# Performance work log

Hardware: AMD Instinct MI355X
Metric: run time of the kernel (lower is better)

## Reference

```python
import jax, jax.numpy as jnp
import numpy as np

N_NODES = 50000
N_EDGES = 800000
IN_DIM = 64
EDGE_DIM = 32
OUT_DIM = 64


def setup_inputs() -> dict:
    key = jax.random.key(0)
    ks = jax.random.split(key, 7)
    x = jax.random.normal(ks[0], (N_NODES, IN_DIM), dtype=jnp.float32)
    edge_index = jax.random.randint(ks[1], (2, N_EDGES), 0, N_NODES, dtype=jnp.int64)
    edge_attr = jax.random.normal(ks[2], (N_EDGES, EDGE_DIM), dtype=jnp.float32)
    scale_msg = 1.0 / np.sqrt(IN_DIM + EDGE_DIM)
    scale_self = 1.0 / np.sqrt(IN_DIM)
    msg_w = jax.random.normal(ks[3], (IN_DIM + EDGE_DIM, OUT_DIM), dtype=jnp.float32) * scale_msg
    msg_b = jax.random.normal(ks[4], (OUT_DIM,), dtype=jnp.float32) * scale_msg
    self_w = jax.random.normal(ks[5], (IN_DIM, OUT_DIM), dtype=jnp.float32) * scale_self
    self_b = jax.random.normal(ks[6], (OUT_DIM,), dtype=jnp.float32) * scale_self
    return {"x": x, "edge_index": edge_index, "edge_attr": edge_attr,
            "msg_w": msg_w, "msg_b": msg_b, "self_w": self_w, "self_b": self_b}


def reference(x, edge_index, edge_attr, msg_w, msg_b, self_w, self_b):
    src = edge_index[0]
    dst = edge_index[1]
    n = x.shape[0]
    # gather source features, concat edge attrs, message linear: [E, out]
    msg_in = jnp.concatenate([x[src], edge_attr], axis=1)
    messages = msg_in @ msg_w + msg_b
    # scatter-mean over destination nodes
    agg = jax.ops.segment_sum(messages, dst, num_segments=n)
    deg = jax.ops.segment_sum(jnp.ones((dst.shape[0],), dtype=x.dtype), dst, num_segments=n)
    deg = jnp.maximum(deg, 1.0)[:, None]
    agg = agg / deg
    return x @ self_w + self_b + agg
```

## Files before the change

### kernel.cpp

```cpp
#include <hip/hip_runtime.h>


constexpr int N_NODES  = 50000;
constexpr int N_EDGES  = 800000;
constexpr int IN_DIM   = 64;
constexpr int EDGE_DIM = 32;
constexpr int OUT_DIM  = 64;
constexpr int CAP      = 48;
constexpr int OVF_CAP  = 65536;

__device__ __forceinline__ void place_one(int dst, int e, int src,
                                          int* cnt, int2* buckets,
                                          int4* ovf, int* ovf_cur) {
    const int pos = atomicAdd(&cnt[dst], 1);
    if (pos < CAP) {
        buckets[(size_t)dst * CAP + pos] = make_int2(e, src);
    } else {
        const int o = atomicAdd(ovf_cur, 1);
        if (o < OVF_CAP) ovf[o] = make_int4(dst, e, src, 0);
    }
}

__global__ __launch_bounds__(256) void place_bucket_k(
    const int* __restrict__ ei, int* cnt, int2* __restrict__ buckets,
    int4* __restrict__ ovf, int* ovf_cur)
{
    const int t = blockIdx.x * 256 + threadIdx.x;
    if (t * 4 + 3 < N_EDGES) {
        const int4 d4 = ((const int4*)(ei + N_EDGES))[t];
        const int4 s4 = ((const int4*)ei)[t];
        place_one(d4.x, 4 * t + 0, s4.x, cnt, buckets, ovf, ovf_cur);
        place_one(d4.y, 4 * t + 1, s4.y, cnt, buckets, ovf, ovf_cur);
        place_one(d4.z, 4 * t + 2, s4.z, cnt, buckets, ovf, ovf_cur);
        place_one(d4.w, 4 * t + 3, s4.w, cnt, buckets, ovf, ovf_cur);
    } else {
        for (int e = t * 4; e < min(t * 4 + 4, N_EDGES); ++e)
            place_one(ei[N_EDGES + e], e, ei[e], cnt, buckets, ovf, ovf_cur);
    }
}

__global__ __launch_bounds__(256) void aggregate_bucket_k(
    const float* __restrict__ x, const float* __restrict__ ea,
    const int2* __restrict__ buckets, const int* __restrict__ cnt,
    const int4* __restrict__ ovf, const int* __restrict__ ovf_cur,
    float* __restrict__ sum_x, float* __restrict__ sum_ea)
{
    const int lane   = threadIdx.x & 63;
    const int wave   = (blockIdx.x * blockDim.x + threadIdx.x) >> 6;
    const int nwaves = (gridDim.x * blockDim.x) >> 6;

    const int grpx = lane >> 4, colx = lane & 15;
    const int grpe = lane >> 3, cole = lane & 7;

    for (int n0 = wave * 2; n0 < N_NODES; n0 += nwaves * 2) {
        const int  nA   = __builtin_amdgcn_readfirstlane(n0);
        const bool hasB = (n0 + 1 < N_NODES);
        const int  nB   = nA + 1;

        const int cFA = __builtin_amdgcn_readfirstlane(cnt[nA]);
        const int cFB = hasB ? __builtin_amdgcn_readfirstlane(cnt[nB]) : 0;
        const int cA  = min(cFA, CAP);
        const int cB  = min(cFB, CAP);

        int eA = 0, srcA = 0, eB = 0, srcB = 0;
        if (lane < cA) { const int2 p = buckets[(size_t)nA * CAP + lane]; eA = p.x; srcA = p.y; }
        if (lane < cB) { const int2 p = buckets[(size_t)nB * CAP + lane]; eB = p.x; srcB = p.y; }

        float4 axA = {0,0,0,0}, aeA = {0,0,0,0};
        float4 axB = {0,0,0,0}, aeB = {0,0,0,0};

        const int mMax = max(cA, cB);
        for (int j = 0; j < mMax; j += 4) {
            const int jj  = j + grpx;
            const int sjA = __shfl(srcA, jj);
            const int sjB = __shfl(srcB, jj);
            if (jj < cA) {
                const float4 v = ((const float4*)(x + (size_t)sjA * IN_DIM))[colx];
                axA.x += v.x; axA.y += v.y; axA.z += v.z; axA.w += v.w;
            }
            if (jj < cB) {
                const float4 v = ((const float4*)(x + (size_t)sjB * IN_DIM))[colx];
                axB.x += v.x; axB.y += v.y; axB.z += v.z; axB.w += v.w;
            }
        }
        for (int j = 0; j < mMax; j += 8) {
            const int jj  = j + grpe;
            const int ejA = __shfl(eA, jj);
            const int ejB = __shfl(eB, jj);
            if (jj < cA) {
                const float4 v = ((const float4*)(ea + (size_t)ejA * EDGE_DIM))[cole];
                aeA.x += v.x; aeA.y += v.y; aeA.z += v.z; aeA.w += v.w;
            }
            if (jj < cB) {
                const float4 v = ((const float4*)(ea + (size_t)ejB * EDGE_DIM))[cole];
                aeB.x += v.x; aeB.y += v.y; aeB.z += v.z; aeB.w += v.w;
            }
        }

        if (cFA > CAP || cFB > CAP) {
            const int novf = min(__builtin_amdgcn_readfirstlane(*ovf_cur), OVF_CAP);
            for (int i = 0; i < novf; ++i) {
                const int4 v = ovf[i];
                const bool mA = (v.x == nA), mB = hasB && (v.x == nB);
                if (mA || mB) {
                    if (grpx == 0) {
                        const float4 t = ((const float4*)(x + (size_t)v.z * IN_DIM))[colx];
                        if (mA) { axA.x += t.x; axA.y += t.y; axA.z += t.z; axA.w += t.w; }
                        else    { axB.x += t.x; axB.y += t.y; axB.z += t.z; axB.w += t.w; }
                    }
                    if (grpe == 0) {
                        const float4 t = ((const float4*)(ea + (size_t)v.y * EDGE_DIM))[cole];
                        if (mA) { aeA.x += t.x; aeA.y += t.y; aeA.z += t.z; aeA.w += t.w; }
                        else    { aeB.x += t.x; aeB.y += t.y; aeB.z += t.z; aeB.w += t.w; }
                    }
                }
            }
        }

#pragma unroll
        for (int mask = 16; mask < 64; mask <<= 1) {
            axA.x += __shfl_xor(axA.x, mask); axA.y += __shfl_xor(axA.y, mask);
            axA.z += __shfl_xor(axA.z, mask); axA.w += __shfl_xor(axA.w, mask);
            axB.x += __shfl_xor(axB.x, mask); axB.y += __shfl_xor(axB.y, mask);
            axB.z += __shfl_xor(axB.z, mask); axB.w += __shfl_xor(axB.w, mask);
        }
#pragma unroll
        for (int mask = 8; mask < 64; mask <<= 1) {
            aeA.x += __shfl_xor(aeA.x, mask); aeA.y += __shfl_xor(aeA.y, mask);
            aeA.z += __shfl_xor(aeA.z, mask); aeA.w += __shfl_xor(aeA.w, mask);
            aeB.x += __shfl_xor(aeB.x, mask); aeB.y += __shfl_xor(aeB.y, mask);
            aeB.z += __shfl_xor(aeB.z, mask); aeB.w += __shfl_xor(aeB.w, mask);
        }

        if (lane < 16) ((float4*)(sum_x + (size_t)nA * IN_DIM))[lane] = axA;
        if (lane < 8)  ((float4*)(sum_ea + (size_t)nA * EDGE_DIM))[lane] = aeA;
        if (hasB) {
            if (lane < 16) ((float4*)(sum_x + (size_t)nB * IN_DIM))[lane] = axB;
            if (lane < 8)  ((float4*)(sum_ea + (size_t)nB * EDGE_DIM))[lane] = aeB;
        }
    }
}

__global__ __launch_bounds__(64) void finalize64_k(
    const float* __restrict__ x, const float* sum_x_in,
    const float* __restrict__ sum_ea, const int* __restrict__ cnt,
    const float* __restrict__ msg_w, const float* __restrict__ msg_b,
    const float* __restrict__ self_w, const float* __restrict__ self_b,
    float* out)
{
    const int c = threadIdx.x;

    float wm[96];
    float wsf[64];
#pragma unroll
    for (int k = 0; k < 96; ++k) wm[k] = msg_w[k * OUT_DIM + c];
#pragma unroll
    for (int k = 0; k < 64; ++k) wsf[k] = self_w[k * OUT_DIM + c];
    const float mb = msg_b[c];
    const float sb = self_b[c];

    for (int n0 = blockIdx.x; n0 < N_NODES; n0 += gridDim.x) {
        const int n = __builtin_amdgcn_readfirstlane(n0);

        const float4* r1 = (const float4*)(sum_x_in + (size_t)n * IN_DIM);
        const float4* r2 = (const float4*)(sum_ea   + (size_t)n * EDGE_DIM);
        const float4* r3 = (const float4*)(x        + (size_t)n * IN_DIM);
        const int d = cnt[n];

        float am0 = 0.f, am1 = 0.f, am2 = 0.f, am3 = 0.f;
        float as0 = 0.f, as1 = 0.f, as2 = 0.f, as3 = 0.f;
#pragma unroll
        for (int q = 0; q < 16; ++q) {
            const float4 v = r1[q];
            am0 = fmaf(v.x, wm[4 * q + 0], am0);
            am1 = fmaf(v.y, wm[4 * q + 1], am1);
            am2 = fmaf(v.z, wm[4 * q + 2], am2);
            am3 = fmaf(v.w, wm[4 * q + 3], am3);
        }
#pragma unroll
        for (int q = 0; q < 8; ++q) {
            const float4 v = r2[q];
            am0 = fmaf(v.x, wm[64 + 4 * q + 0], am0);
            am1 = fmaf(v.y, wm[64 + 4 * q + 1], am1);
            am2 = fmaf(v.z, wm[64 + 4 * q + 2], am2);
            am3 = fmaf(v.w, wm[64 + 4 * q + 3], am3);
        }
#pragma unroll
        for (int q = 0; q < 16; ++q) {
            const float4 v = r3[q];
            as0 = fmaf(v.x, wsf[4 * q + 0], as0);
            as1 = fmaf(v.y, wsf[4 * q + 1], as1);
            as2 = fmaf(v.z, wsf[4 * q + 2], as2);
            as3 = fmaf(v.w, wsf[4 * q + 3], as3);
        }

        const float inv  = 1.0f / (float)max(d, 1);
        const float bsel = (d > 0) ? 1.0f : 0.0f;
        const float am   = (am0 + am1) + (am2 + am3);
        const float as   = (as0 + as1) + (as2 + as3);

        out[(size_t)n * OUT_DIM + c] = as + sb + am * inv + mb * bsel;
    }
}

__global__ __launch_bounds__(768) void scatter_fb_k(
    const float* __restrict__ x, const int* __restrict__ ei,
    const float* __restrict__ ea, float* sum_x, float* sum_ea, int* deg)
{
    const int t  = threadIdx.x;
    const int el = t / 96;
    const int k  = t - el * 96;
    const int e  = blockIdx.x * 8 + el;
    if (e >= N_EDGES) return;
    const int dst = ei[N_EDGES + e];
    if (k < IN_DIM) {
        const int src = ei[e];
        atomicAdd(&sum_x[dst * IN_DIM + k], x[src * IN_DIM + k]);
        if (k == 0) atomicAdd(&deg[dst], 1);
    } else {
        const int kk = k - IN_DIM;
        atomicAdd(&sum_ea[dst * EDGE_DIM + kk], ea[e * EDGE_DIM + kk]);
    }
}

extern "C" void kernel_launch(void* const* d_in, const int* in_sizes, int n_in,
                              void* d_out, int out_size, void* d_ws, size_t ws_size,
                              hipStream_t stream) {
    const float* x      = (const float*)d_in[0];
    const int*   ei     = (const int*)d_in[1];
    const float* ea     = (const float*)d_in[2];
    const float* msg_w  = (const float*)d_in[3];
    const float* msg_b  = (const float*)d_in[4];
    const float* self_w = (const float*)d_in[5];
    const float* self_b = (const float*)d_in[6];

    float* out = (float*)d_out;

    int*   cnt     = (int*)d_ws;
    int*   ovf_cur = cnt + N_NODES;
    int2*  buckets = (int2*)(cnt + N_NODES + 16);
    int4*  ovf     = (int4*)(buckets + (size_t)N_NODES * CAP);
    float* sum_ea  = (float*)(ovf + OVF_CAP);
    const size_t need_bucket =
        ((size_t)N_NODES + 16 + 2 * (size_t)N_NODES * CAP + 4 * (size_t)OVF_CAP +
         (size_t)N_NODES * EDGE_DIM) * sizeof(int);

    if (ws_size >= need_bucket) {
        hipMemsetAsync(cnt, 0, (N_NODES + 16) * sizeof(int), stream);
        place_bucket_k<<<(N_EDGES / 4 + 255) / 256, 256, 0, stream>>>(
            ei, cnt, buckets, ovf, ovf_cur);
        aggregate_bucket_k<<<(N_NODES / 2 + 3) / 4, 256, 0, stream>>>(
            x, ea, buckets, cnt, ovf, ovf_cur, out, sum_ea);
        finalize64_k<<<4096, 64, 0, stream>>>(
            x, out, sum_ea, cnt, msg_w, msg_b, self_w, self_b, out);
    } else {
        float* fb_sum_ea = (float*)d_ws;
        int*   deg       = (int*)(fb_sum_ea + (size_t)N_NODES * EDGE_DIM);
        hipMemsetAsync(d_out, 0, (size_t)N_NODES * OUT_DIM * sizeof(float), stream);
        hipMemsetAsync(d_ws, 0, (size_t)N_NODES * (EDGE_DIM + 1) * sizeof(float), stream);
        scatter_fb_k<<<(N_EDGES + 7) / 8, 768, 0, stream>>>(
            x, ei, ea, out, fb_sum_ea, deg);
        finalize64_k<<<4096, 64, 0, stream>>>(
            x, out, fb_sum_ea, deg, msg_w, msg_b, self_w, self_b, out);
    }
}
```

Before: 299.3 us.

## Restructure aggregation to one node per wave with batched gathers, prefetch in finalize

```diff
diff --git a/kernel.cpp b/kernel.cpp
--- a/kernel.cpp
+++ b/kernel.cpp
@@ -8,6 +8,13 @@
 constexpr int OUT_DIM  = 64;
 constexpr int CAP      = 48;
 constexpr int OVF_CAP  = 65536;
+
+using vf4 = __attribute__((ext_vector_type(4))) float;
+using vi2 = __attribute__((ext_vector_type(2))) int;
+
+__device__ __forceinline__ float rl(float v, int srclane) {
+    return __int_as_float(__builtin_amdgcn_readlane(__float_as_int(v), srclane));
+}
 
 __device__ __forceinline__ void place_one(int dst, int e, int src,
                                           int* cnt, int2* buckets,
@@ -39,167 +46,190 @@
     }
 }
 
-__global__ __launch_bounds__(256) void aggregate_bucket_k(
+__global__ __launch_bounds__(256) void aggregate1_k(
     const float* __restrict__ x, const float* __restrict__ ea,
     const int2* __restrict__ buckets, const int* __restrict__ cnt,
     const int4* __restrict__ ovf, const int* __restrict__ ovf_cur,
     float* __restrict__ sum_x, float* __restrict__ sum_ea)
 {
-    const int lane   = threadIdx.x & 63;
-    const int wave   = (blockIdx.x * blockDim.x + threadIdx.x) >> 6;
-    const int nwaves = (gridDim.x * blockDim.x) >> 6;
+    const int lane = threadIdx.x & 63;
+    const int wave = (blockIdx.x * blockDim.x + threadIdx.x) >> 6;
+    if (wave >= N_NODES) return;
+    const int n = __builtin_amdgcn_readfirstlane(wave);
+
+    const vi2 p = __builtin_nontemporal_load(
+        (const vi2*)buckets + (size_t)n * CAP + lane);
+    const int cF = __builtin_amdgcn_readfirstlane(cnt[n]);
+    const int c  = min(cF, CAP);
+    const int e0 = p.x, s0 = p.y;
 
     const int grpx = lane >> 4, colx = lane & 15;
     const int grpe = lane >> 3, cole = lane & 7;
 
-    for (int n0 = wave * 2; n0 < N_NODES; n0 += nwaves * 2) {
-        const int  nA   = __builtin_amdgcn_readfirstlane(n0);
-        const bool hasB = (n0 + 1 < N_NODES);
-        const int  nB   = nA + 1;
-
-        const int cFA = __builtin_amdgcn_readfirstlane(cnt[nA]);
-        const int cFB = hasB ? __builtin_amdgcn_readfirstlane(cnt[nB]) : 0;
-        const int cA  = min(cFA, CAP);
-        const int cB  = min(cFB, CAP);
-
-        int eA = 0, srcA = 0, eB = 0, srcB = 0;
-        if (lane < cA) { const int2 p = buckets[(size_t)nA * CAP + lane]; eA = p.x; srcA = p.y; }
-        if (lane < cB) { const int2 p = buckets[(size_t)nB * CAP + lane]; eB = p.x; srcB = p.y; }
-
-        float4 axA = {0,0,0,0}, aeA = {0,0,0,0};
-        float4 axB = {0,0,0,0}, aeB = {0,0,0,0};
-
-        const int mMax = max(cA, cB);
-        for (int j = 0; j < mMax; j += 4) {
-            const int jj  = j + grpx;
-            const int sjA = __shfl(srcA, jj);
-            const int sjB = __shfl(srcB, jj);
-            if (jj < cA) {
-                const float4 v = ((const float4*)(x + (size_t)sjA * IN_DIM))[colx];
-                axA.x += v.x; axA.y += v.y; axA.z += v.z; axA.w += v.w;
+    vf4 xt[12], et[6];
+#pragma unroll
+    for (int i = 0; i < 12; ++i) xt[i] = (vf4){0, 0, 0, 0};
+#pragma unroll
+    for (int i = 0; i < 6; ++i) et[i] = (vf4){0, 0, 0, 0};
+
+#pragma unroll
+    for (int i = 0; i < 4; ++i) {
+        const int jj = 4 * i + grpx;
+        const int s  = __shfl(s0, jj);
+        if (jj < c) xt[i] = ((const vf4*)(x + (size_t)s * IN_DIM))[colx];
+    }
+#pragma unroll
+    for (int i = 0; i < 2; ++i) {
+        const int jj = 8 * i + grpe;
+        const int e  = __shfl(e0, jj);
+        if (jj < c) et[i] = __builtin_nontemporal_load(
+            (const vf4*)(ea + (size_t)e * EDGE_DIM) + cole);
+    }
+    if (c > 16) {
+#pragma unroll
+        for (int i = 4; i < 8; ++i) {
+            const int jj = 4 * i + grpx;
+            const int s  = __shfl(s0, jj);
+            if (jj < c) xt[i] = ((const vf4*)(x + (size_t)s * IN_DIM))[colx];
+        }
+#pragma unroll
+        for (int i = 2; i < 4; ++i) {
+            const int jj = 8 * i + grpe;
+            const int e  = __shfl(e0, jj);
+            if (jj < c) et[i] = __builtin_nontemporal_load(
+                (const vf4*)(ea + (size_t)e * EDGE_DIM) + cole);
+        }
+    }
+    if (c > 32) {
+#pragma unroll
+        for (int i = 8; i < 12; ++i) {
+            const int jj = 4 * i + grpx;
+            const int s  = __shfl(s0, jj);
+            if (jj < c) xt[i] = ((const vf4*)(x + (size_t)s * IN_DIM))[colx];
+        }
+#pragma unroll
+        for (int i = 4; i < 6; ++i) {
+            const int jj = 8 * i + grpe;
+            const int e  = __shfl(e0, jj);
+            if (jj < c) et[i] = __builtin_nontemporal_load(
+                (const vf4*)(ea + (size_t)e * EDGE_DIM) + cole);
+        }
+    }
+
+    vf4 ax = ((xt[0] + xt[1]) + (xt[2] + xt[3])) +
+             ((xt[4] + xt[5]) + (xt[6] + xt[7])) +
+             ((xt[8] + xt[9]) + (xt[10] + xt[11]));
+    vf4 ae = ((et[0] + et[1]) + (et[2] + et[3])) + (et[4] + et[5]);
+
+    if (cF > CAP) {
+        const int novf = min(__builtin_amdgcn_readfirstlane(*ovf_cur), OVF_CAP);
+        for (int i = 0; i < novf; ++i) {
+            const int4 v = ovf[i];
+            if (v.x == n) {
+                if (grpx == 0)
+                    ax += ((const vf4*)(x + (size_t)v.z * IN_DIM))[colx];
+                if (grpe == 0)
+                    ae += ((const vf4*)(ea + (size_t)v.y * EDGE_DIM))[cole];
             }
-            if (jj < cB) {
-                const float4 v = ((const float4*)(x + (size_t)sjB * IN_DIM))[colx];
-                axB.x += v.x; axB.y += v.y; axB.z += v.z; axB.w += v.w;
-            }
-        }
-        for (int j = 0; j < mMax; j += 8) {
-            const int jj  = j + grpe;
-            const int ejA = __shfl(eA, jj);
-            const int ejB = __shfl(eB, jj);
-            if (jj < cA) {
-                const float4 v = ((const float4*)(ea + (size_t)ejA * EDGE_DIM))[cole];
-                aeA.x += v.x; aeA.y += v.y; aeA.z += v.z; aeA.w += v.w;
-            }
-            if (jj < cB) {
-                const float4 v = ((const float4*)(ea + (size_t)ejB * EDGE_DIM))[cole];
-                aeB.x += v.x; aeB.y += v.y; aeB.z += v.z; aeB.w += v.w;
-            }
-        }
-
-        if (cFA > CAP || cFB > CAP) {
-            const int novf = min(__builtin_amdgcn_readfirstlane(*ovf_cur), OVF_CAP);
-            for (int i = 0; i < novf; ++i) {
-                const int4 v = ovf[i];
-                const bool mA = (v.x == nA), mB = hasB && (v.x == nB);
-                if (mA || mB) {
-                    if (grpx == 0) {
-                        const float4 t = ((const float4*)(x + (size_t)v.z * IN_DIM))[colx];
-                        if (mA) { axA.x += t.x; axA.y += t.y; axA.z += t.z; axA.w += t.w; }
-                        else    { axB.x += t.x; axB.y += t.y; axB.z += t.z; axB.w += t.w; }
-                    }
-                    if (grpe == 0) {
-                        const float4 t = ((const float4*)(ea + (size_t)v.y * EDGE_DIM))[cole];
-                        if (mA) { aeA.x += t.x; aeA.y += t.y; aeA.z += t.z; aeA.w += t.w; }
-                        else    { aeB.x += t.x; aeB.y += t.y; aeB.z += t.z; aeB.w += t.w; }
-                    }
-                }
-            }
-        }
-
-#pragma unroll
-        for (int mask = 16; mask < 64; mask <<= 1) {
-            axA.x += __shfl_xor(axA.x, mask); axA.y += __shfl_xor(axA.y, mask);
-            axA.z += __shfl_xor(axA.z, mask); axA.w += __shfl_xor(axA.w, mask);
-            axB.x += __shfl_xor(axB.x, mask); axB.y += __shfl_xor(axB.y, mask);
-            axB.z += __shfl_xor(axB.z, mask); axB.w += __shfl_xor(axB.w, mask);
-        }
-#pragma unroll
-        for (int mask = 8; mask < 64; mask <<= 1) {
-            aeA.x += __shfl_xor(aeA.x, mask); aeA.y += __shfl_xor(aeA.y, mask);
-            aeA.z += __shfl_xor(aeA.z, mask); aeA.w += __shfl_xor(aeA.w, mask);
-            aeB.x += __shfl_xor(aeB.x, mask); aeB.y += __shfl_xor(aeB.y, mask);
-            aeB.z += __shfl_xor(aeB.z, mask); aeB.w += __shfl_xor(aeB.w, mask);
-        }
-
-        if (lane < 16) ((float4*)(sum_x + (size_t)nA * IN_DIM))[lane] = axA;
-        if (lane < 8)  ((float4*)(sum_ea + (size_t)nA * EDGE_DIM))[lane] = aeA;
-        if (hasB) {
-            if (lane < 16) ((float4*)(sum_x + (size_t)nB * IN_DIM))[lane] = axB;
-            if (lane < 8)  ((float4*)(sum_ea + (size_t)nB * EDGE_DIM))[lane] = aeB;
-        }
-    }
-}
-
-__global__ __launch_bounds__(64) void finalize64_k(
+        }
+    }
+
+#pragma unroll
+    for (int mask = 16; mask < 64; mask <<= 1) {
+        ax.x += __shfl_xor(ax.x, mask); ax.y += __shfl_xor(ax.y, mask);
+        ax.z += __shfl_xor(ax.z, mask); ax.w += __shfl_xor(ax.w, mask);
+    }
+#pragma unroll
+    for (int mask = 8; mask < 64; mask <<= 1) {
+        ae.x += __shfl_xor(ae.x, mask); ae.y += __shfl_xor(ae.y, mask);
+        ae.z += __shfl_xor(ae.z, mask); ae.w += __shfl_xor(ae.w, mask);
+    }
+
+    if (lane < 16) ((vf4*)(sum_x + (size_t)n * IN_DIM))[lane] = ax;
+    if (lane < 8)  ((vf4*)(sum_ea + (size_t)n * EDGE_DIM))[lane] = ae;
+}
+
+__device__ __forceinline__ void fin_load_node(
+    const float* x, const float* sum_x_in, const float* sum_ea,
+    const int* cnt, int n, int lane,
+    vf4& r1, vf4& r2, vf4& r3, int& d)
+{
+    r1 = (vf4){0, 0, 0, 0}; r2 = (vf4){0, 0, 0, 0}; r3 = (vf4){0, 0, 0, 0};
+    if (lane < 16) {
+        r1 = ((const vf4*)(sum_x_in + (size_t)n * IN_DIM))[lane];
+        r3 = ((const vf4*)(x        + (size_t)n * IN_DIM))[lane];
+    }
+    if (lane < 8) r2 = ((const vf4*)(sum_ea + (size_t)n * EDGE_DIM))[lane];
+    d = cnt[n];
+}
+
+__global__ __launch_bounds__(256, 2) void finalize_v4_k(
     const float* __restrict__ x, const float* sum_x_in,
     const float* __restrict__ sum_ea, const int* __restrict__ cnt,
     const float* __restrict__ msg_w, const float* __restrict__ msg_b,
     const float* __restrict__ self_w, const float* __restrict__ self_b,
     float* out)
 {
-    const int c = threadIdx.x;
+    const int lane = threadIdx.x & 63;
+    const int wid  = blockIdx.x * 4 + (threadIdx.x >> 6);
+    const int nw   = gridDim.x * 4;
 
     float wm[96];
     float wsf[64];
 #pragma unroll
-    for (int k = 0; k < 96; ++k) wm[k] = msg_w[k * OUT_DIM + c];
-#pragma unroll
-    for (int k = 0; k < 64; ++k) wsf[k] = self_w[k * OUT_DIM + c];
-    const float mb = msg_b[c];
-    const float sb = self_b[c];
-
-    for (int n0 = blockIdx.x; n0 < N_NODES; n0 += gridDim.x) {
-        const int n = __builtin_amdgcn_readfirstlane(n0);
-
-        const float4* r1 = (const float4*)(sum_x_in + (size_t)n * IN_DIM);
-        const float4* r2 = (const float4*)(sum_ea   + (size_t)n * EDGE_DIM);
-        const float4* r3 = (const float4*)(x        + (size_t)n * IN_DIM);
-        const int d = cnt[n];
+    for (int k = 0; k < 96; ++k) wm[k] = msg_w[k * OUT_DIM + lane];
+#pragma unroll
+    for (int k = 0; k < 64; ++k) wsf[k] = self_w[k * OUT_DIM + lane];
+    const float mb = msg_b[lane];
+    const float sb = self_b[lane];
+
+    int n = wid;
+    if (n >= N_NODES) return;
+
+    vf4 r1, r2, r3; int d;
+    fin_load_node(x, sum_x_in, sum_ea, cnt,
+                  __builtin_amdgcn_readfirstlane(n), lane, r1, r2, r3, d);
+
+    while (true) {
+        const int n1 = n + nw;
+        vf4 q1 = {0,0,0,0}, q2 = {0,0,0,0}, q3 = {0,0,0,0}; int d1 = 0;
+        if (n1 < N_NODES)
+            fin_load_node(x, sum_x_in, sum_ea, cnt,
+                          __builtin_amdgcn_readfirstlane(n1), lane,
+                          q1, q2, q3, d1);
 
         float am0 = 0.f, am1 = 0.f, am2 = 0.f, am3 = 0.f;
         float as0 = 0.f, as1 = 0.f, as2 = 0.f, as3 = 0.f;
 #pragma unroll
         for (int q = 0; q < 16; ++q) {
-            const float4 v = r1[q];
-            am0 = fmaf(v.x, wm[4 * q + 0], am0);
-            am1 = fmaf(v.y, wm[4 * q + 1], am1);
-            am2 = fmaf(v.z, wm[4 * q + 2], am2);
-            am3 = fmaf(v.w, wm[4 * q + 3], am3);
+            am0 = fmaf(rl(r1[0], q), wm[4 * q + 0], am0);
+            am1 = fmaf(rl(r1[1], q), wm[4 * q + 1], am1);
+            am2 = fmaf(rl(r1[2], q), wm[4 * q + 2], am2);
+            am3 = fmaf(rl(r1[3], q), wm[4 * q + 3], am3);
         }
 #pragma unroll
         for (int q = 0; q < 8; ++q) {
-            const float4 v = r2[q];
-            am0 = fmaf(v.x, wm[64 + 4 * q + 0], am0);
-            am1 = fmaf(v.y, wm[64 + 4 * q + 1], am1);
-            am2 = fmaf(v.z, wm[64 + 4 * q + 2], am2);
-            am3 = fmaf(v.w, wm[64 + 4 * q + 3], am3);
+            am0 = fmaf(rl(r2[0], q), wm[64 + 4 * q + 0], am0);
+            am1 = fmaf(rl(r2[1], q), wm[64 + 4 * q + 1], am1);
+            am2 = fmaf(rl(r2[2], q), wm[64 + 4 * q + 2], am2);
+            am3 = fmaf(rl(r2[3], q), wm[64 + 4 * q + 3], am3);
         }
 #pragma unroll
         for (int q = 0; q < 16; ++q) {
-            const float4 v = r3[q];
-            as0 = fmaf(v.x, wsf[4 * q + 0], as0);
-            as1 = fmaf(v.y, wsf[4 * q + 1], as1);
-            as2 = fmaf(v.z, wsf[4 * q + 2], as2);
-            as3 = fmaf(v.w, wsf[4 * q + 3], as3);
+            as0 = fmaf(rl(r3[0], q), wsf[4 * q + 0], as0);
+            as1 = fmaf(rl(r3[1], q), wsf[4 * q + 1], as1);
+            as2 = fmaf(rl(r3[2], q), wsf[4 * q + 2], as2);
+            as3 = fmaf(rl(r3[3], q), wsf[4 * q + 3], as3);
         }
 
         const float inv  = 1.0f / (float)max(d, 1);
         const float bsel = (d > 0) ? 1.0f : 0.0f;
-        const float am   = (am0 + am1) + (am2 + am3);
-        const float as   = (as0 + as1) + (as2 + as3);
-
-        out[(size_t)n * OUT_DIM + c] = as + sb + am * inv + mb * bsel;
+        out[(size_t)n * OUT_DIM + lane] =
+            ((as0 + as1) + (as2 + as3)) + sb +
+            ((am0 + am1) + (am2 + am3)) * inv + mb * bsel;
+
+        if (n1 >= N_NODES) break;
+        n = n1; r1 = q1; r2 = q2; r3 = q3; d = d1;
     }
 }
 
@@ -249,9 +279,9 @@
         hipMemsetAsync(cnt, 0, (N_NODES + 16) * sizeof(int), stream);
         place_bucket_k<<<(N_EDGES / 4 + 255) / 256, 256, 0, stream>>>(
             ei, cnt, buckets, ovf, ovf_cur);
-        aggregate_bucket_k<<<(N_NODES / 2 + 3) / 4, 256, 0, stream>>>(
+        aggregate1_k<<<(N_NODES + 3) / 4, 256, 0, stream>>>(
             x, ea, buckets, cnt, ovf, ovf_cur, out, sum_ea);
-        finalize64_k<<<4096, 64, 0, stream>>>(
+        finalize_v4_k<<<512, 256, 0, stream>>>(
             x, out, sum_ea, cnt, msg_w, msg_b, self_w, self_b, out);
     } else {
         float* fb_sum_ea = (float*)d_ws;
@@ -260,7 +290,7 @@
         hipMemsetAsync(d_ws, 0, (size_t)N_NODES * (EDGE_DIM + 1) * sizeof(float), stream);
         scatter_fb_k<<<(N_EDGES + 7) / 8, 768, 0, stream>>>(
             x, ei, ea, out, fb_sum_ea, deg);
-        finalize64_k<<<4096, 64, 0, stream>>>(
+        finalize_v4_k<<<512, 256, 0, stream>>>(
             x, out, fb_sum_ea, deg, msg_w, msg_b, self_w, self_b, out);
     }
 }
```

Result: slower. 331.4 us (+10.7%).
